# Kernel tuning notes

Measured on AMD Instinct MI355X. Metric: run time of the kernel, lower is better.

## Reference

```python
import jax, jax.numpy as jnp
import numpy as np

B, SEQ, F = 256, 2048, 5
IN1, U1, U2 = SEQ * F, 32, 1
UNFOLDS = 6          # ODE solver unfolds per cell call
ELAPSED = 1.0        # elapsed time per call


def _cell_params(key, n_in, n_u):
    ks = jax.random.split(key, 9)
    U = lambda k, shp, lo, hi: jax.random.uniform(k, shp, jnp.float32, lo, hi)
    return dict(
        input_w=jnp.ones((n_in,), jnp.float32),
        input_b=jnp.zeros((n_in,), jnp.float32),
        smu=U(ks[0], (n_in, n_u), 0.3, 0.8),
        ssig=U(ks[1], (n_in, n_u), 3.0, 8.0),
        sW=U(ks[2], (n_in, n_u), 0.001, 1.0),
        serev=2.0 * jax.random.bernoulli(ks[3], 0.5, (n_in, n_u)).astype(jnp.float32) - 1.0,
        mu=U(ks[4], (n_u, n_u), 0.3, 0.8),
        sig=U(ks[5], (n_u, n_u), 3.0, 8.0),
        W=U(ks[6], (n_u, n_u), 0.001, 1.0),
        erev=2.0 * jax.random.bernoulli(ks[7], 0.5, (n_u, n_u)).astype(jnp.float32) - 1.0,
        gleak=jnp.ones((n_u,), jnp.float32),
        vleak=U(ks[8], (n_u,), -0.2, 0.2),
        cm=0.5 * jnp.ones((n_u,), jnp.float32),
    )


def setup_inputs() -> dict:
    key = jax.random.key(0)
    kx, ka, kb = jax.random.split(key, 3)
    inp = {"x": jax.random.normal(kx, (B, SEQ, F), jnp.float32)}
    for pfx, k, n_in, n_u in (("a_", ka, IN1, U1), ("b_", kb, U1, U2)):
        for name, v in _cell_params(k, n_in, n_u).items():
            inp[pfx + name] = v
    return inp


def _ltc(x, iw, ib, smu, ssig, sW, serev, mu, sig, W, erev, gleak, vleak, cm):
    # x: [B, n_in]; input affine mapping
    x = x * iw + ib
    # sensory synapse activations: [B, n_in, n_u]
    sact = sW * jax.nn.sigmoid((x[:, :, None] - smu) * ssig)
    w_num_s = jnp.einsum('biu,iu->bu', sact, serev)   # reversal-weighted sum
    w_den_s = jnp.sum(sact, axis=1)
    cm_t = cm / (ELAPSED / UNFOLDS)                   # [n_u]
    v0 = jnp.zeros((x.shape[0], cm.shape[0]), x.dtype)

    def body(v, _):
        # recurrent synapses: presyn axis 1, postsyn axis 2 -> [B, n_u, n_u]
        wact = W * jax.nn.sigmoid((v[:, :, None] - mu) * sig)
        num = cm_t * v + gleak * vleak + jnp.einsum('bij,ij->bj', wact, erev) + w_num_s
        den = cm_t + gleak + jnp.sum(wact, axis=1) + w_den_s
        return num / den, None

    v, _ = jax.lax.scan(body, v0, None, length=UNFOLDS)
    return v


def reference(x,
              a_input_w, a_input_b, a_smu, a_ssig, a_sW, a_serev,
              a_mu, a_sig, a_W, a_erev, a_gleak, a_vleak, a_cm,
              b_input_w, b_input_b, b_smu, b_ssig, b_sW, b_serev,
              b_mu, b_sig, b_W, b_erev, b_gleak, b_vleak, b_cm):
    bsz = x.shape[0]
    xb = x.reshape(bsz, -1)  # [B, seq*5]
    h = _ltc(xb, a_input_w, a_input_b, a_smu, a_ssig, a_sW, a_serev,
             a_mu, a_sig, a_W, a_erev, a_gleak, a_vleak, a_cm)     # [B, 32]
    h2 = _ltc(h, b_input_w, b_input_b, b_smu, b_ssig, b_sW, b_serev,
              b_mu, b_sig, b_W, b_erev, b_gleak, b_vleak, b_cm)    # [B, 1]
    return jax.nn.sigmoid(h2).reshape(bsz)
```

## Files before the change

### kernel.cpp

```cpp
#include <hip/hip_runtime.h>

#define BATCH 256
#define IN1   10240
#define NU    32
#define NB    32
#define BGROUPS (BATCH / NB)
#define TILE_I 80
#define XPAD   84
#define LOG2E 1.4426950408889634f

__global__ __launch_bounds__(256) void ltc_sensory_partial(
    const float* __restrict__ x,
    const float* __restrict__ iw, const float* __restrict__ ibias,
    const float* __restrict__ smu, const float* __restrict__ ssig,
    const float* __restrict__ sW, const float* __restrict__ serev,
    float2* __restrict__ part, int stripe)
{
    const int tid = threadIdx.x;
    const int u   = tid & 31;
    const int il  = tid >> 5;
    const int wv  = tid >> 6;
    const int b0  = blockIdx.x * NB;
    const int ibase = blockIdx.y * stripe;
    const int iend  = (ibase + stripe < IN1) ? (ibase + stripe) : IN1;

    union SmemT {
        float xL[NB][XPAD];
        float wred[4][NB][NU][2];
    };
    __shared__ SmemT sm;

    float accn[NB], accd[NB];
#pragma unroll
    for (int n = 0; n < NB; ++n) { accn[n] = 0.f; accd[n] = 0.f; }

    const int lrow = tid >> 3;
    const int lq   = tid & 7;

    for (int cb = ibase; cb < iend; cb += TILE_I) {
        const int cend = (cb + TILE_I < iend) ? (cb + TILE_I) : iend;
        const int cw   = cend - cb;
        __syncthreads();
        const float* xrow = x + (size_t)(b0 + lrow) * IN1 + cb;
        for (int c4 = lq; c4 * 4 < cw; c4 += 8) {
            if (c4 * 4 + 3 < cw) {
                const float4 v4 = *(const float4*)(xrow + c4 * 4);
                *(float4*)&sm.xL[lrow][c4 * 4] = v4;
            } else {
                for (int t = c4 * 4; t < cw; ++t)
                    sm.xL[lrow][t] = xrow[t];
            }
        }
        __syncthreads();

        for (int i = cb + il; i < cend; i += 8) {
            const int pi = i * NU + u;
            float A = ssig[pi] * LOG2E;
            const float C = (smu[pi] - ibias[i]) * A;
            A *= iw[i];
            const float sw  = sW[pi];
            const float swe = sw * serev[pi];
            const float* xr = &sm.xL[0][0] + (i - cb);
#pragma unroll
            for (int n = 0; n < NB; ++n) {
                const float xv = xr[n * XPAD];
                const float e  = __builtin_amdgcn_exp2f(C - xv * A);
                const float r  = __builtin_amdgcn_rcpf(1.0f + e);
                accd[n] = fmaf(sw,  r, accd[n]);
                accn[n] = fmaf(swe, r, accn[n]);
            }
        }
    }

    __syncthreads();
#pragma unroll
    for (int n = 0; n < NB; ++n) {
        float vn = accn[n] + __shfl_xor(accn[n], 32, 64);
        float vd = accd[n] + __shfl_xor(accd[n], 32, 64);
        if ((tid & 63) < 32) {
            sm.wred[wv][n][u][0] = vn;
            sm.wred[wv][n][u][1] = vd;
        }
    }
    __syncthreads();
    for (int p = tid; p < NB * NU; p += 256) {
        const int n = p >> 5, uu = p & 31;
        const float sn = sm.wred[0][n][uu][0] + sm.wred[1][n][uu][0]
                       + sm.wred[2][n][uu][0] + sm.wred[3][n][uu][0];
        const float sd = sm.wred[0][n][uu][1] + sm.wred[1][n][uu][1]
                       + sm.wred[2][n][uu][1] + sm.wred[3][n][uu][1];
        part[((size_t)blockIdx.y * BATCH + (b0 + n)) * NU + uu] =
            make_float2(sn, sd);
    }
}

__global__ __launch_bounds__(256) void ltc_reduce(
    const float2* __restrict__ part, int nsplit, float2* __restrict__ S)
{
    const int tid = threadIdx.x;
    const int b   = blockIdx.x;
    const int u   = tid & 31;
    const int sl  = tid >> 5;

    __shared__ float sred[8][NU][2];

    float sn = 0.f, sd = 0.f;
#pragma unroll 4
    for (int s = sl; s < nsplit; s += 8) {
        const float2 p = part[((size_t)s * BATCH + b) * NU + u];
        sn += p.x;
        sd += p.y;
    }
    sred[sl][u][0] = sn;
    sred[sl][u][1] = sd;
    __syncthreads();

    if (tid >= 32) return;
    float Sn = 0.f, Sd = 0.f;
#pragma unroll
    for (int s2 = 0; s2 < 8; ++s2) {
        Sn += sred[s2][u][0];
        Sd += sred[s2][u][1];
    }
    S[(size_t)b * NU + u] = make_float2(Sn, Sd);
}

__global__ __launch_bounds__(256) void ltc_unfold(
    const float2* __restrict__ S,
    const float* __restrict__ amu, const float* __restrict__ asig,
    const float* __restrict__ aW,  const float* __restrict__ aerev,
    const float* __restrict__ agleak, const float* __restrict__ avleak,
    const float* __restrict__ acm,
    const float* __restrict__ b_iw, const float* __restrict__ b_ib,
    const float* __restrict__ b_smu, const float* __restrict__ b_ssig,
    const float* __restrict__ b_sW,  const float* __restrict__ b_serev,
    const float* __restrict__ b_mu,  const float* __restrict__ b_sig,
    const float* __restrict__ b_W,   const float* __restrict__ b_erev,
    const float* __restrict__ b_gleak, const float* __restrict__ b_vleak,
    const float* __restrict__ b_cm,
    float* __restrict__ out)
{
    const int tid = threadIdx.x;
    const int u   = tid & 31;
    const int bl  = tid >> 5;
    const int b   = blockIdx.x * 8 + bl;

    __shared__ float pAp[NU*NU], pCp[NU*NU];
    __shared__ float pW[NU*NU],  pWE[NU*NU];

    for (int p = tid; p < NU * NU; p += 256) {
        const float sg = asig[p] * LOG2E;
        pAp[p] = sg;
        pCp[p] = amu[p] * sg;
        const float w = aW[p];
        pW[p]  = w;
        pWE[p] = w * aerev[p];
    }
    __syncthreads();

    const float2 Sv = S[(size_t)b * NU + u];
    const float Sn = Sv.x, Sd = Sv.y;

    const float cmt = acm[u] * 6.0f;
    const float gl  = agleak[u];
    const float gv  = gl * avleak[u];

    float v = 0.f;
    for (int k = 0; k < 6; ++k) {
        float rn = 0.f, rd = 0.f;
#pragma unroll
        for (int j = 0; j < NU; ++j) {
            const float vj = __shfl(v, j, 32);
            const int pi = j * NU + u;
            const float e = __builtin_amdgcn_exp2f(pCp[pi] - vj * pAp[pi]);
            const float r = __builtin_amdgcn_rcpf(1.0f + e);
            rn = fmaf(pWE[pi], r, rn);
            rd = fmaf(pW[pi],  r, rd);
        }
        const float num = cmt * v + gv + rn + Sn;
        const float den = cmt + gl + rd + Sd;
        v = num / den;
    }

    const float x2  = v * b_iw[u] + b_ib[u];
    const float e2  = __builtin_amdgcn_exp2f((b_smu[u] - x2) * b_ssig[u] * LOG2E);
    const float s2v = b_sW[u] * __builtin_amdgcn_rcpf(1.0f + e2);
    float wn = s2v * b_serev[u];
    float wd = s2v;
#pragma unroll
    for (int m = 16; m >= 1; m >>= 1) {
        wn += __shfl_xor(wn, m, 32);
        wd += __shfl_xor(wd, m, 32);
    }

    const float bcmt = b_cm[0] * 6.0f;
    const float bgl  = b_gleak[0];
    const float bgv  = bgl * b_vleak[0];
    const float bmu  = b_mu[0], bsig = b_sig[0], bW = b_W[0], berev = b_erev[0];
    float v2 = 0.f;
#pragma unroll
    for (int k = 0; k < 6; ++k) {
        const float ee = __builtin_amdgcn_exp2f((bmu - v2) * bsig * LOG2E);
        const float ws = bW * __builtin_amdgcn_rcpf(1.0f + ee);
        const float num = bcmt * v2 + bgv + ws * berev + wn;
        const float den = bcmt + bgl + ws + wd;
        v2 = num / den;
    }

    if (u == 0)
        out[b] = 1.0f / (1.0f + __builtin_amdgcn_exp2f(-v2 * LOG2E));
}

extern "C" void kernel_launch(void* const* d_in, const int* in_sizes, int n_in,
                              void* d_out, int out_size, void* d_ws, size_t ws_size,
                              hipStream_t stream) {
    const float* x       = (const float*)d_in[0];
    const float* a_iw    = (const float*)d_in[1];
    const float* a_ib    = (const float*)d_in[2];
    const float* a_smu   = (const float*)d_in[3];
    const float* a_ssig  = (const float*)d_in[4];
    const float* a_sW    = (const float*)d_in[5];
    const float* a_serev = (const float*)d_in[6];
    const float* a_mu    = (const float*)d_in[7];
    const float* a_sig   = (const float*)d_in[8];
    const float* a_W     = (const float*)d_in[9];
    const float* a_erev  = (const float*)d_in[10];
    const float* a_gleak = (const float*)d_in[11];
    const float* a_vleak = (const float*)d_in[12];
    const float* a_cm    = (const float*)d_in[13];
    const float* b_iw    = (const float*)d_in[14];
    const float* b_ib    = (const float*)d_in[15];
    const float* b_smu   = (const float*)d_in[16];
    const float* b_ssig  = (const float*)d_in[17];
    const float* b_sW    = (const float*)d_in[18];
    const float* b_serev = (const float*)d_in[19];
    const float* b_mu    = (const float*)d_in[20];
    const float* b_sig   = (const float*)d_in[21];
    const float* b_W     = (const float*)d_in[22];
    const float* b_erev  = (const float*)d_in[23];
    const float* b_gleak = (const float*)d_in[24];
    const float* b_vleak = (const float*)d_in[25];
    const float* b_cm    = (const float*)d_in[26];
    float* out = (float*)d_out;

    int splits = 128;
    while (splits > 1 &&
           ((size_t)splits * BATCH * NU + BATCH * NU) * sizeof(float2) > ws_size)
        splits >>= 1;
    int stripe = (IN1 + splits - 1) / splits;
    stripe = (stripe + 7) & ~7;
    const int gy = (IN1 + stripe - 1) / stripe;

    float2* part = (float2*)d_ws;
    float2* S    = part + (size_t)splits * BATCH * NU;

    dim3 grid1(BGROUPS, gy);
    ltc_sensory_partial<<<grid1, 256, 0, stream>>>(
        x, a_iw, a_ib, a_smu, a_ssig, a_sW, a_serev, part, stripe);

    ltc_reduce<<<BATCH, 256, 0, stream>>>(part, gy, S);

    ltc_unfold<<<BATCH / 8, 256, 0, stream>>>(
        S,
        a_mu, a_sig, a_W, a_erev, a_gleak, a_vleak, a_cm,
        b_iw, b_ib, b_smu, b_ssig, b_sW, b_serev,
        b_mu, b_sig, b_W, b_erev, b_gleak, b_vleak, b_cm,
        out);
}
```

Before: 49.91 us.

## Restructure sensory kernel: per-thread batch rows, shared param tiles, more splits

The sensory partial kernel now precomputes per-chunk synapse parameters (scale, offset, weight, weighted reversal) into shared memory as float4s, and each thread accumulates 4 batch rows across all inputs of the chunk instead of 32 rows over a strided input subset. This removes the cross-wave shared-memory reduction at the end and cuts register pressure from 64 accumulators to 8. The split count rises to 256 so more blocks fill the GPU, at the cost of a larger partial buffer for the reduce kernel. Stripe boundaries now assume IN1 divides evenly by splits and CHUNK, so the tail handling is gone.

```diff
diff --git a/kernel.cpp b/kernel.cpp
--- a/kernel.cpp
+++ b/kernel.cpp
@@ -5,8 +5,8 @@
 #define NU    32
 #define NB    32
 #define BGROUPS (BATCH / NB)
-#define TILE_I 80
-#define XPAD   84
+#define CHUNK 40
+#define XPAD  44
 #define LOG2E 1.4426950408889634f
 
 __global__ __launch_bounds__(256) void ltc_sensory_partial(
@@ -18,79 +18,64 @@
 {
     const int tid = threadIdx.x;
     const int u   = tid & 31;
-    const int il  = tid >> 5;
-    const int wv  = tid >> 6;
+    const int g   = tid >> 5;
     const int b0  = blockIdx.x * NB;
     const int ibase = blockIdx.y * stripe;
-    const int iend  = (ibase + stripe < IN1) ? (ibase + stripe) : IN1;
-
-    union SmemT {
-        float xL[NB][XPAD];
-        float wred[4][NB][NU][2];
-    };
-    __shared__ SmemT sm;
-
-    float accn[NB], accd[NB];
-#pragma unroll
-    for (int n = 0; n < NB; ++n) { accn[n] = 0.f; accd[n] = 0.f; }
+    const int iend  = ibase + stripe;
+
+    __shared__ float4 sP[CHUNK * NU];
+    __shared__ float  xL[NB][XPAD];
+
+    float accn[4], accd[4];
+#pragma unroll
+    for (int k = 0; k < 4; ++k) { accn[k] = 0.f; accd[k] = 0.f; }
 
     const int lrow = tid >> 3;
     const int lq   = tid & 7;
 
-    for (int cb = ibase; cb < iend; cb += TILE_I) {
-        const int cend = (cb + TILE_I < iend) ? (cb + TILE_I) : iend;
-        const int cw   = cend - cb;
+    for (int cb = ibase; cb < iend; cb += CHUNK) {
         __syncthreads();
+
+#pragma unroll
+        for (int p = tid; p < CHUNK * NU; p += 256) {
+            const int ii = cb + (p >> 5);
+            const int gi = ii * NU + (p & 31);
+            const float sg = ssig[gi] * LOG2E;
+            const float w  = sW[gi];
+            sP[p] = make_float4(sg * iw[ii],
+                                (smu[gi] - ibias[ii]) * sg,
+                                w, w * serev[gi]);
+        }
         const float* xrow = x + (size_t)(b0 + lrow) * IN1 + cb;
-        for (int c4 = lq; c4 * 4 < cw; c4 += 8) {
-            if (c4 * 4 + 3 < cw) {
-                const float4 v4 = *(const float4*)(xrow + c4 * 4);
-                *(float4*)&sm.xL[lrow][c4 * 4] = v4;
-            } else {
-                for (int t = c4 * 4; t < cw; ++t)
-                    sm.xL[lrow][t] = xrow[t];
+        {
+            const float4 v4 = *(const float4*)(xrow + lq * 4);
+            *(float4*)&xL[lrow][lq * 4] = v4;
+            if (lq < 2) {
+                const float4 w4 = *(const float4*)(xrow + (lq + 8) * 4);
+                *(float4*)&xL[lrow][(lq + 8) * 4] = w4;
             }
         }
         __syncthreads();
 
-        for (int i = cb + il; i < cend; i += 8) {
-            const int pi = i * NU + u;
-            float A = ssig[pi] * LOG2E;
-            const float C = (smu[pi] - ibias[i]) * A;
-            A *= iw[i];
-            const float sw  = sW[pi];
-            const float swe = sw * serev[pi];
-            const float* xr = &sm.xL[0][0] + (i - cb);
-#pragma unroll
-            for (int n = 0; n < NB; ++n) {
-                const float xv = xr[n * XPAD];
-                const float e  = __builtin_amdgcn_exp2f(C - xv * A);
+        const float* xr = &xL[g * 4][0];
+#pragma unroll 2
+        for (int di = 0; di < CHUNK; ++di) {
+            const float4 f = sP[di * NU + u];
+#pragma unroll
+            for (int k = 0; k < 4; ++k) {
+                const float xv = xr[k * XPAD + di];
+                const float e  = __builtin_amdgcn_exp2f(f.y - xv * f.x);
                 const float r  = __builtin_amdgcn_rcpf(1.0f + e);
-                accd[n] = fmaf(sw,  r, accd[n]);
-                accn[n] = fmaf(swe, r, accn[n]);
+                accd[k] = fmaf(f.z, r, accd[k]);
+                accn[k] = fmaf(f.w, r, accn[k]);
             }
         }
     }
 
-    __syncthreads();
-#pragma unroll
-    for (int n = 0; n < NB; ++n) {
-        float vn = accn[n] + __shfl_xor(accn[n], 32, 64);
-        float vd = accd[n] + __shfl_xor(accd[n], 32, 64);
-        if ((tid & 63) < 32) {
-            sm.wred[wv][n][u][0] = vn;
-            sm.wred[wv][n][u][1] = vd;
-        }
-    }
-    __syncthreads();
-    for (int p = tid; p < NB * NU; p += 256) {
-        const int n = p >> 5, uu = p & 31;
-        const float sn = sm.wred[0][n][uu][0] + sm.wred[1][n][uu][0]
-                       + sm.wred[2][n][uu][0] + sm.wred[3][n][uu][0];
-        const float sd = sm.wred[0][n][uu][1] + sm.wred[1][n][uu][1]
-                       + sm.wred[2][n][uu][1] + sm.wred[3][n][uu][1];
-        part[((size_t)blockIdx.y * BATCH + (b0 + n)) * NU + uu] =
-            make_float2(sn, sd);
+#pragma unroll
+    for (int k = 0; k < 4; ++k) {
+        part[((size_t)blockIdx.y * BATCH + (b0 + g * 4 + k)) * NU + u] =
+            make_float2(accn[k], accd[k]);
     }
 }
 
@@ -105,7 +90,7 @@
     __shared__ float sred[8][NU][2];
 
     float sn = 0.f, sd = 0.f;
-#pragma unroll 4
+#pragma unroll 8
     for (int s = sl; s < nsplit; s += 8) {
         const float2 p = part[((size_t)s * BATCH + b) * NU + u];
         sn += p.x;
@@ -243,22 +228,20 @@
     const float* b_cm    = (const float*)d_in[26];
     float* out = (float*)d_out;
 
-    int splits = 128;
-    while (splits > 1 &&
+    int splits = 256;
+    while (splits > 4 &&
            ((size_t)splits * BATCH * NU + BATCH * NU) * sizeof(float2) > ws_size)
         splits >>= 1;
-    int stripe = (IN1 + splits - 1) / splits;
-    stripe = (stripe + 7) & ~7;
-    const int gy = (IN1 + stripe - 1) / stripe;
+    const int stripe = IN1 / splits;
 
     float2* part = (float2*)d_ws;
     float2* S    = part + (size_t)splits * BATCH * NU;
 
-    dim3 grid1(BGROUPS, gy);
+    dim3 grid1(BGROUPS, splits);
     ltc_sensory_partial<<<grid1, 256, 0, stream>>>(
         x, a_iw, a_ib, a_smu, a_ssig, a_sW, a_serev, part, stripe);
 
-    ltc_reduce<<<BATCH, 256, 0, stream>>>(part, gy, S);
+    ltc_reduce<<<BATCH, 256, 0, stream>>>(part, splits, S);
 
     ltc_unfold<<<BATCH / 8, 256, 0, stream>>>(
         S,
```

New measurement: 45.08 us. 9.7% less time.
